# Performance work log

Measured on AMD Instinct MI355X. Metric: run time of the kernel, lower is better.

## Reference

```python
import jax, jax.numpy as jnp
import numpy as np

D_INSTR, D_ACT, D_OBJ, TOK = 768, 7, 256, 256


def setup_inputs() -> dict:
    key = jax.random.key(0)
    ks = jax.random.split(key, 10)
    B, NDEMO, NOBJ = 256, 16, 64
    inp = {
        "instr_embedding": jax.random.normal(ks[0], (B, D_INSTR), jnp.float32),
        "demo_object_embeddings": jax.random.normal(ks[1], (NDEMO, B, NOBJ, D_OBJ), jnp.float32),
        "demo_actions": jax.random.normal(ks[2], (NDEMO, B, D_ACT), jnp.float32),
        "current_object_embeddings": jax.random.normal(ks[3], (B, NOBJ, D_OBJ), jnp.float32),
        # learned params (stored as (in, out); equivalent math to torch Linear)
        "W_instr": jax.random.normal(ks[4], (D_INSTR, TOK), jnp.float32) / np.sqrt(D_INSTR),
        "b_instr": jax.random.normal(ks[5], (TOK,), jnp.float32) * 0.01,
        "W_act": jax.random.normal(ks[6], (D_ACT, TOK), jnp.float32) / np.sqrt(D_ACT),
        "b_act": jax.random.normal(ks[7], (TOK,), jnp.float32) * 0.01,
        "W_obj": jax.random.normal(ks[8], (D_OBJ, TOK), jnp.float32) / np.sqrt(D_OBJ),
        "b_obj": jax.random.normal(ks[9], (TOK,), jnp.float32) * 0.01,
    }
    return inp


def reference(instr_embedding, demo_object_embeddings, demo_actions,
              current_object_embeddings, W_instr, b_instr, W_act, b_act,
              W_obj, b_obj):
    # Project everything in single batched GEMMs (structure is uniform across batch,
    # so the per-example Python loop in the original collapses to dense ops).
    instr_tok = instr_embedding @ W_instr + b_instr            # (B, T)
    demo_obj_tok = jnp.einsum('dbnf,ft->dbnt', demo_object_embeddings, W_obj) + b_obj  # (D,B,No,T)
    act_tok = jnp.einsum('dbf,ft->dbt', demo_actions, W_act) + b_act                   # (D,B,T)
    cur_tok = jnp.einsum('bnf,ft->bnt', current_object_embeddings, W_obj) + b_obj      # (B,No,T)

    D, B, No, T = demo_obj_tok.shape
    # Per demo: [objects..., action] -> (D, B, No+1, T), then interleave demos in order.
    demo_block = jnp.concatenate([demo_obj_tok, act_tok[:, :, None, :]], axis=2)
    demo_block = demo_block.transpose(1, 0, 2, 3).reshape(B, D * (No + 1), T)
    # Final sequence: [instr, demo1_objs, demo1_action, ..., current_objs]
    return jnp.concatenate([instr_tok[:, None, :], demo_block, cur_tok], axis=1)
```

## Files before the change

### kernel.cpp

```cpp
#include <hip/hip_runtime.h>
#include <hip/hip_bf16.h>
#include <stdint.h>

#define TOK   256
#define NOBJ  64
#define NDEMO 16
#define BATCH 256
#define SEQ   1105
#define NDG   (NDEMO * BATCH)
#define NGRP  (NDG + BATCH)
#define NHT   (NGRP * 2)
#define NG    8
#define OBJ_BLKS   (NHT / NG)
#define ACT_BLKS   512
#define INSTR_BLKS 128
#define TOTAL_BLKS (ACT_BLKS + INSTR_BLKS + OBJ_BLKS)

typedef __bf16 bf16x8 __attribute__((ext_vector_type(8)));
typedef float  f32x4  __attribute__((ext_vector_type(4)));

static __device__ __forceinline__ unsigned pack_bf16x2(float a, float b) {
    unsigned ua = __float_as_uint(a);
    unsigned ub = __float_as_uint(b);
    unsigned ra = (ua + 0x7FFFu + ((ua >> 16) & 1u)) >> 16;
    unsigned rb = (ub + 0x7FFFu + ((ub >> 16) & 1u)) >> 16;
    return (ra & 0xFFFFu) | (rb << 16);
}

static __device__ __forceinline__ uint16_t f32_to_bf16_bits(float a) {
    unsigned ua = __float_as_uint(a);
    return (uint16_t)((ua + 0x7FFFu + ((ua >> 16) & 1u)) >> 16);
}

static __device__ __forceinline__ bf16x8 pack8(float4 lo, float4 hi) {
    union { uint4 u; bf16x8 b; } r;
    r.u.x = pack_bf16x2(lo.x, lo.y);
    r.u.y = pack_bf16x2(lo.z, lo.w);
    r.u.z = pack_bf16x2(hi.x, hi.y);
    r.u.w = pack_bf16x2(hi.z, hi.w);
    return r.b;
}

static __device__ __forceinline__ void gload_lds16(const float* g, void* l) {
    __builtin_amdgcn_global_load_lds(
        (const __attribute__((address_space(1))) uint32_t*)g,
        (__attribute__((address_space(3))) uint32_t*)l,
        16, 0, 0);
}

__global__ void wconv_frag_kernel(const float* __restrict__ W, uint16_t* __restrict__ Wf) {
    int q = blockIdx.x * 256 + threadIdx.x;
    int lane = q & 63;
    int s  = (q >> 6) & 7;
    int j  = (q >> 9) & 3;
    int wc = (q >> 11) & 3;
    int tcol = wc * 64 + j * 16 + (lane & 15);
    int k0   = s * 32 + (lane >> 4) * 8;
    uint4 w;
    unsigned p[4];
#pragma unroll
    for (int h = 0; h < 4; ++h) {
        float a = W[(size_t)(k0 + 2 * h)     * TOK + tcol];
        float b = W[(size_t)(k0 + 2 * h + 1) * TOK + tcol];
        p[h] = pack_bf16x2(a, b);
    }
    w.x = p[0]; w.y = p[1]; w.z = p[2]; w.w = p[3];
    *reinterpret_cast<uint4*>(Wf + (size_t)q * 8) = w;
}

__global__ __launch_bounds__(256, 2) void fused_kernel(
    const float* __restrict__ demo_obj,
    const float* __restrict__ cur,
    const float* __restrict__ b_obj,
    const __bf16* __restrict__ Wf,
    const float* __restrict__ demo_act,
    const float* __restrict__ W_act,
    const float* __restrict__ b_act,
    const float* __restrict__ instr,
    const float* __restrict__ W_instr,
    const float* __restrict__ b_instr,
    float* __restrict__ out)
{
    __shared__ __align__(16) float lds[2 * 32 * TOK];
    int blk = blockIdx.x;
    int tid = threadIdx.x;

    if (blk >= ACT_BLKS + INSTR_BLKS) {
        int ob = blk - (ACT_BLKS + INSTR_BLKS);
        int h0 = ob * NG;
        const float* base = (h0 < 2 * NDG)
            ? demo_obj + (size_t)h0 * (32 * TOK)
            : cur + (size_t)(h0 - 2 * NDG) * (32 * TOK);

        int wave = tid >> 6, lane = tid & 63;
        int l15 = lane & 15, l4 = lane >> 4;
        int n0 = wave * 64;

        auto STAGE = [&](int it, int bsel) {
            const float* sb = base + (size_t)it * (32 * TOK);
            float* dst = lds + bsel * (32 * TOK);
#pragma unroll
            for (int i = 0; i < 8; ++i) {
                int r = i * 4 + wave;
                int gch = r * 64 + (lane ^ (r & 7));
                gload_lds16(sb + (size_t)gch * 4, dst + (size_t)(i * 256 + tid) * 4);
            }
        };

        bf16x8 wf[4][8];
        {
            const __bf16* fb = Wf + ((size_t)wave * 32 * 64 + lane) * 8;
#pragma unroll
            for (int j = 0; j < 4; ++j)
#pragma unroll
                for (int s = 0; s < 8; ++s)
                    wf[j][s] = *reinterpret_cast<const bf16x8*>(fb + (size_t)(j * 8 + s) * 64 * 8);
        }
#pragma unroll
        for (int j = 0; j < 4; ++j)
#pragma unroll
            for (int s = 0; s < 8; ++s)
                asm volatile("" : "+v"(wf[j][s]));

        f32x4 bv4[4];
#pragma unroll
        for (int j = 0; j < 4; ++j)
            bv4[j] = *reinterpret_cast<const f32x4*>(b_obj + n0 + j * 16 + l4 * 4);

        STAGE(0, 0);
        STAGE(1, 1);

#pragma unroll 1
        for (int it = 0; it < NG; ++it) {
            asm volatile("s_waitcnt vmcnt(8)" ::: "memory");
            __builtin_amdgcn_s_barrier();
            __builtin_amdgcn_sched_barrier(0);

            if (it + 1 < NG) STAGE(it + 1, (it + 1) & 1);

            const float* buf = lds + (it & 1) * (32 * TOK);

            f32x4 acc[2][4];
#pragma unroll
            for (int i = 0; i < 2; ++i)
#pragma unroll
                for (int j = 0; j < 4; ++j) {
                    f32x4 z = {0.0f, 0.0f, 0.0f, 0.0f};
                    acc[i][j] = z;
                }

#pragma unroll
            for (int s = 0; s < 8; ++s) {
                bf16x8 a[2];
#pragma unroll
                for (int i = 0; i < 2; ++i) {
                    int r = i * 16 + l15;
                    int c0 = s * 8 + l4 * 2;
                    float4 lo = *reinterpret_cast<const float4*>(buf + r * TOK + ((c0 ^ (r & 7)) * 4));
                    float4 hi = *reinterpret_cast<const float4*>(buf + r * TOK + (((c0 + 1) ^ (r & 7)) * 4));
                    a[i] = pack8(lo, hi);
                }
#pragma unroll
                for (int j = 0; j < 4; ++j) {
                    acc[0][j] = __builtin_amdgcn_mfma_f32_16x16x32_bf16(wf[j][s], a[0], acc[0][j], 0, 0, 0);
                    acc[1][j] = __builtin_amdgcn_mfma_f32_16x16x32_bf16(wf[j][s], a[1], acc[1][j], 0, 0, 0);
                }
            }

            int h = h0 + it;
            int gg = h >> 1, half = h & 1;
            int row_base;
            if (h < 2 * NDG) {
                int d = gg >> 8, b = gg & 255;
                row_base = b * SEQ + 1 + d * (NOBJ + 1) + half * 32;
            } else {
                int b = gg - NDG;
                row_base = b * SEQ + 1 + NDEMO * (NOBJ + 1) + half * 32;
            }
#pragma unroll
            for (int i = 0; i < 2; ++i) {
                int row = row_base + i * 16 + l15;
#pragma unroll
                for (int j = 0; j < 4; ++j) {
                    f32x4 v = acc[i][j] + bv4[j];
                    *reinterpret_cast<f32x4*>(out + (size_t)row * TOK + n0 + j * 16 + l4 * 4) = v;
                }
            }
        }

    } else if (blk < ACT_BLKS) {
        int g8 = blk * 8;
        int t = tid;
        float v[8];
        float bb = b_act[t];
#pragma unroll
        for (int r = 0; r < 8; ++r) v[r] = bb;
#pragma unroll
        for (int k = 0; k < 7; ++k) {
            float wv = W_act[k * TOK + t];
#pragma unroll
            for (int r = 0; r < 8; ++r)
                v[r] += demo_act[(size_t)(g8 + r) * 7 + k] * wv;
        }
#pragma unroll
        for (int r = 0; r < 8; ++r) {
            int g = g8 + r;
            int d = g >> 8, b = g & 255;
            out[(size_t)(b * SEQ + (d + 1) * (NOBJ + 1)) * TOK + t] = v[r];
        }

    } else {
        int b0 = (blk - ACT_BLKS) * 2;
        int t = tid;
        float* buf = lds;
        const float* src = instr + (size_t)b0 * 768;
#pragma unroll
        for (int i = 0; i < 6; ++i) buf[i * 256 + t] = src[i * 256 + t];
        __syncthreads();
        float a0 = b_instr[t], a1 = a0;
#pragma unroll 4
        for (int k = 0; k < 768; ++k) {
            float wv = W_instr[(size_t)k * TOK + t];
            a0 += buf[k] * wv;
            a1 += buf[768 + k] * wv;
        }
        out[(size_t)b0 * SEQ * TOK + t] = a0;
        out[(size_t)(b0 + 1) * SEQ * TOK + t] = a1;
    }
}

extern "C" void kernel_launch(void* const* d_in, const int* in_sizes, int n_in,
                              void* d_out, int out_size, void* d_ws, size_t ws_size,
                              hipStream_t stream) {
    (void)in_sizes; (void)n_in; (void)out_size; (void)ws_size;
    const float* instr    = (const float*)d_in[0];
    const float* demo_obj = (const float*)d_in[1];
    const float* demo_act = (const float*)d_in[2];
    const float* cur      = (const float*)d_in[3];
    const float* W_instr  = (const float*)d_in[4];
    const float* b_instr  = (const float*)d_in[5];
    const float* W_act    = (const float*)d_in[6];
    const float* b_act    = (const float*)d_in[7];
    const float* W_obj    = (const float*)d_in[8];
    const float* b_obj    = (const float*)d_in[9];
    float* out = (float*)d_out;

    uint16_t* Wf = (uint16_t*)d_ws;

    wconv_frag_kernel<<<32, 256, 0, stream>>>(W_obj, Wf);
    fused_kernel<<<TOTAL_BLKS, 256, 0, stream>>>(
        demo_obj, cur, b_obj, (const __bf16*)d_ws,
        demo_act, W_act, b_act, instr, W_instr, b_instr, out);
}
```

Before: 157.4 us.

## Convert staged fp32 tile to swizzled bf16 LDS buffer once per iteration

The object-GEMM path now stages each fp32 tile into a single LDS buffer. All threads convert it cooperatively to bf16 into a double-buffered, XOR-swizzled bf16 region, then the next fp32 tile load is issued. The MFMA A-fragments become one 16-byte LDS read each instead of two fp32 reads plus per-lane packing, which removes redundant conversion work across the four waves. The cost is an extra barrier and LDS round trip per iteration. Loads also overlap less, because only one fp32 buffer exists and the next load waits until conversion finishes.

```diff
diff --git a/kernel.cpp b/kernel.cpp
--- a/kernel.cpp
+++ b/kernel.cpp
@@ -27,20 +27,6 @@
     return (ra & 0xFFFFu) | (rb << 16);
 }
 
-static __device__ __forceinline__ uint16_t f32_to_bf16_bits(float a) {
-    unsigned ua = __float_as_uint(a);
-    return (uint16_t)((ua + 0x7FFFu + ((ua >> 16) & 1u)) >> 16);
-}
-
-static __device__ __forceinline__ bf16x8 pack8(float4 lo, float4 hi) {
-    union { uint4 u; bf16x8 b; } r;
-    r.u.x = pack_bf16x2(lo.x, lo.y);
-    r.u.y = pack_bf16x2(lo.z, lo.w);
-    r.u.z = pack_bf16x2(hi.x, hi.y);
-    r.u.w = pack_bf16x2(hi.z, hi.w);
-    return r.b;
-}
-
 static __device__ __forceinline__ void gload_lds16(const float* g, void* l) {
     __builtin_amdgcn_global_load_lds(
         (const __attribute__((address_space(1))) uint32_t*)g,
@@ -81,7 +67,8 @@
     const float* __restrict__ b_instr,
     float* __restrict__ out)
 {
-    __shared__ __align__(16) float lds[2 * 32 * TOK];
+    __shared__ __align__(16) unsigned char lds_raw[65536];
+    float* F = reinterpret_cast<float*>(lds_raw);
     int blk = blockIdx.x;
     int tid = threadIdx.x;
 
@@ -96,15 +83,12 @@
         int l15 = lane & 15, l4 = lane >> 4;
         int n0 = wave * 64;
 
-        auto STAGE = [&](int it, int bsel) {
+        auto STAGE = [&](int it) {
             const float* sb = base + (size_t)it * (32 * TOK);
-            float* dst = lds + bsel * (32 * TOK);
-#pragma unroll
-            for (int i = 0; i < 8; ++i) {
-                int r = i * 4 + wave;
-                int gch = r * 64 + (lane ^ (r & 7));
-                gload_lds16(sb + (size_t)gch * 4, dst + (size_t)(i * 256 + tid) * 4);
-            }
+#pragma unroll
+            for (int i = 0; i < 8; ++i)
+                gload_lds16(sb + (size_t)(i * 256 + tid) * 4,
+                            F + (size_t)(i * 256 + tid) * 4);
         };
 
         bf16x8 wf[4][8];
@@ -124,22 +108,44 @@
 
         f32x4 bv4[4];
 #pragma unroll
-        for (int j = 0; j < 4; ++j)
+        for (int j = 0; j < 4; ++j) {
             bv4[j] = *reinterpret_cast<const f32x4*>(b_obj + n0 + j * 16 + l4 * 4);
-
-        STAGE(0, 0);
-        STAGE(1, 1);
+            asm volatile("" : "+v"(bv4[j]));
+        }
+
+        STAGE(0);
 
 #pragma unroll 1
         for (int it = 0; it < NG; ++it) {
-            asm volatile("s_waitcnt vmcnt(8)" ::: "memory");
+            if (it == 0) asm volatile("s_waitcnt vmcnt(0)" ::: "memory");
+            else         asm volatile("s_waitcnt vmcnt(8)" ::: "memory");
             __builtin_amdgcn_s_barrier();
             __builtin_amdgcn_sched_barrier(0);
 
-            if (it + 1 < NG) STAGE(it + 1, (it + 1) & 1);
-
-            const float* buf = lds + (it & 1) * (32 * TOK);
-
+            __bf16* B = reinterpret_cast<__bf16*>(lds_raw + 32768 + (it & 1) * 16384);
+#pragma unroll
+            for (int i = 0; i < 4; ++i) {
+                int p = i * 256 + tid;
+                int row = p >> 5;
+                int c8  = p & 31;
+                float4 lo = *reinterpret_cast<const float4*>(F + (size_t)p * 8);
+                float4 hi = *reinterpret_cast<const float4*>(F + (size_t)p * 8 + 4);
+                bf16x8 o;
+                o[0] = (__bf16)lo.x; o[1] = (__bf16)lo.y;
+                o[2] = (__bf16)lo.z; o[3] = (__bf16)lo.w;
+                o[4] = (__bf16)hi.x; o[5] = (__bf16)hi.y;
+                o[6] = (__bf16)hi.z; o[7] = (__bf16)hi.w;
+                unsigned off = (unsigned)(row * 512 + c8 * 16) ^ (unsigned)((row & 7) << 4);
+                *reinterpret_cast<bf16x8*>(reinterpret_cast<unsigned char*>(B) + off) = o;
+            }
+            asm volatile("s_waitcnt lgkmcnt(0)" ::: "memory");
+            __builtin_amdgcn_sched_barrier(0);
+            __builtin_amdgcn_s_barrier();
+            __builtin_amdgcn_sched_barrier(0);
+
+            if (it + 1 < NG) STAGE(it + 1);
+
+            const unsigned char* Bb = lds_raw + 32768 + (it & 1) * 16384;
             f32x4 acc[2][4];
 #pragma unroll
             for (int i = 0; i < 2; ++i)
@@ -155,10 +161,8 @@
 #pragma unroll
                 for (int i = 0; i < 2; ++i) {
                     int r = i * 16 + l15;
-                    int c0 = s * 8 + l4 * 2;
-                    float4 lo = *reinterpret_cast<const float4*>(buf + r * TOK + ((c0 ^ (r & 7)) * 4));
-                    float4 hi = *reinterpret_cast<const float4*>(buf + r * TOK + (((c0 + 1) ^ (r & 7)) * 4));
-                    a[i] = pack8(lo, hi);
+                    unsigned off = (unsigned)(r * 512 + s * 64 + l4 * 16) ^ (unsigned)((r & 7) << 4);
+                    a[i] = *reinterpret_cast<const bf16x8*>(Bb + off);
                 }
 #pragma unroll
                 for (int j = 0; j < 4; ++j) {
@@ -212,7 +216,7 @@
     } else {
         int b0 = (blk - ACT_BLKS) * 2;
         int t = tid;
-        float* buf = lds;
+        float* buf = F;
         const float* src = instr + (size_t)b0 * 768;
 #pragma unroll
         for (int i = 0; i < 6; ++i) buf[i * 256 + t] = src[i * 256 + t];
```

After: 157.2 us. No clear change (-0.1%).
